# Performance work log

Hardware: AMD Instinct MI355X
Metric: run time of the kernel (lower is better)

## Reference

```python
import jax, jax.numpy as jnp
import numpy as np

B, N1, N2, D = 2, 512, 512, 128


def setup_inputs() -> dict:
    key = jax.random.key(0)
    ks = jax.random.split(key, 7)
    return {
        "x0": jax.random.normal(ks[0], (B, N1, D), dtype=jnp.float32),
        "x": jax.random.normal(ks[1], (B, N1, D), dtype=jnp.float32),
        "y": jax.random.normal(ks[2], (B, N2, D), dtype=jnp.float32),
        "W1": jax.random.normal(ks[3], (3 * D, D), dtype=jnp.float32) * (1.0 / np.sqrt(3 * D)),
        "b1": jax.random.normal(ks[4], (D,), dtype=jnp.float32) * 0.02,
        "W2": jax.random.normal(ks[5], (D, 1), dtype=jnp.float32) * (1.0 / np.sqrt(D)),
        "b2": jax.random.normal(ks[6], (1,), dtype=jnp.float32) * 0.02,
    }


def reference(x0, x, y, W1, b1, W2, b2):
    # linear1(concat([x0, x, y], -1)) == x0 @ W1[:D] + x @ W1[D:2D] + y @ W1[2D:] + b1
    d = x.shape[-1]
    Wa, Wb, Wc = W1[:d], W1[d:2 * d], W1[2 * d:]
    # small GEMMs on the un-expanded operands, then broadcast-add over the pair grid
    hx = jnp.einsum('bnd,de->bne', x0, Wa) + jnp.einsum('bnd,de->bne', x, Wb)  # [b, n1, d]
    hy = jnp.einsum('bmd,de->bme', y, Wc)                                      # [b, n2, d]
    h = hx[:, :, None, :] + hy[:, None, :, :] + b1                             # [b, n1, n2, d]
    h = jax.nn.gelu(h, approximate=False)                                      # torch nn.GELU default (erf)
    o = jnp.einsum('bnme,eo->bnmo', h, W2) + b2                                # [b, n1, n2, 1]
    return o[..., 0]                                                           # [b, n1, n2]
```

## Files before the change

kernel.cpp:

```cpp
#include <hip/hip_runtime.h>

#define BB 2
#define NN1 512
#define NN2 512
#define DD 128
#define TS 32
#define SXPAD 132

struct GeluPoly {
    float p[10];
    constexpr GeluPoly() : p{} {
        const int N = 10;
        const double PI = 3.14159265358979323846;
        double fv[10] = {};
        double xv[10] = {};
        for (int j = 0; j < N; ++j) {
            double th = PI * (j + 0.5) / N;
            double cth = 1.0, term = 1.0, t2 = th * th;
            for (int k = 1; k <= 30; ++k) {
                term *= -t2 / ((2.0 * k - 1.0) * (2.0 * k));
                cth += term;
            }
            xv[j] = cth;
            double t = 4.5 * (cth + 1.0);
            double s = t > 1.0 ? t : 1.0;
            for (int it = 0; it < 64; ++it) s = 0.5 * (s + t / s);
            double x = s * 0.70710678118654752440;
            double esum = 0.0, pw = x, fact = 1.0;
            for (int k = 0; k < 48; ++k) {
                if (k > 0) { fact *= (double)k; pw *= x * x; }
                double tk = pw / (fact * (2.0 * k + 1.0));
                esum += (k & 1) ? -tk : tk;
            }
            double erfv = 1.12837916709551257390 * esum;
            fv[j] = 0.5 * erfv / s;
        }
        double ck[10] = {};
        for (int k = 0; k < N; ++k) {
            double sum = 0.0;
            for (int j = 0; j < N; ++j) {
                double Tk = 1.0;
                if (k >= 1) {
                    double Tm2 = 1.0, Tm1 = xv[j];
                    Tk = xv[j];
                    for (int i = 2; i <= k; ++i) {
                        Tk = 2.0 * xv[j] * Tm1 - Tm2;
                        Tm2 = Tm1; Tm1 = Tk;
                    }
                }
                sum += fv[j] * Tk;
            }
            ck[k] = 2.0 * sum / N;
        }
        ck[0] *= 0.5;
        double T[10][10] = {};
        T[0][0] = 1.0;
        T[1][1] = 1.0;
        for (int k = 2; k < N; ++k)
            for (int i = 0; i < N; ++i)
                T[k][i] = 2.0 * (i > 0 ? T[k - 1][i - 1] : 0.0) - T[k - 2][i];
        double pd[10] = {};
        for (int k = 0; k < N; ++k)
            for (int i = 0; i < N; ++i)
                pd[i] += ck[k] * T[k][i];
        for (int i = 0; i < N; ++i) p[i] = (float)pd[i];
    }
};
static constexpr GeluPoly GP{};

__device__ __forceinline__ float gelu_poly(float s) {
    float c = __builtin_amdgcn_fmed3f(s, -3.0f, 3.0f);
    float t = c * c;
    float u = __builtin_fmaf(t, 0.22222222222222222f, -1.0f);
    float q = GP.p[9];
    #pragma unroll
    for (int k = 8; k >= 0; --k) q = __builtin_fmaf(q, u, GP.p[k]);
    float phi = __builtin_fmaf(c, q, 0.5f);
    return s * phi;
}

#define PR 8
__global__ __launch_bounds__(256) void proj_kernel(
    const float* __restrict__ x0, const float* __restrict__ x,
    const float* __restrict__ y,  const float* __restrict__ W1,
    const float* __restrict__ b1, float* __restrict__ hx, float* __restrict__ hy) {
    const int e = threadIdx.x & (DD - 1);
    const int g = threadIdx.x >> 7;
    const int nxb = (BB * NN1) / PR;
    const float* Wa = W1;
    const float* Wb = W1 + DD * DD;
    const float* Wc = W1 + 2 * DD * DD;

    if (blockIdx.x < nxb) {
        const int row0 = blockIdx.x * PR + g * (PR / 2);
        float acc0 = b1[e], acc1 = b1[e], acc2 = b1[e], acc3 = b1[e];
        #pragma unroll 4
        for (int d = 0; d < DD; ++d) {
            const float wa = Wa[d * DD + e];
            const float wb = Wb[d * DD + e];
            acc0 += x0[(row0 + 0) * DD + d] * wa + x[(row0 + 0) * DD + d] * wb;
            acc1 += x0[(row0 + 1) * DD + d] * wa + x[(row0 + 1) * DD + d] * wb;
            acc2 += x0[(row0 + 2) * DD + d] * wa + x[(row0 + 2) * DD + d] * wb;
            acc3 += x0[(row0 + 3) * DD + d] * wa + x[(row0 + 3) * DD + d] * wb;
        }
        hx[(row0 + 0) * DD + e] = acc0;
        hx[(row0 + 1) * DD + e] = acc1;
        hx[(row0 + 2) * DD + e] = acc2;
        hx[(row0 + 3) * DD + e] = acc3;
    } else {
        const int row0 = (blockIdx.x - nxb) * PR + g * (PR / 2);
        float acc0 = 0.f, acc1 = 0.f, acc2 = 0.f, acc3 = 0.f;
        #pragma unroll 4
        for (int d = 0; d < DD; ++d) {
            const float wc = Wc[d * DD + e];
            acc0 += y[(row0 + 0) * DD + d] * wc;
            acc1 += y[(row0 + 1) * DD + d] * wc;
            acc2 += y[(row0 + 2) * DD + d] * wc;
            acc3 += y[(row0 + 3) * DD + d] * wc;
        }
        hy[(row0 + 0) * DD + e] = acc0;
        hy[(row0 + 1) * DD + e] = acc1;
        hy[(row0 + 2) * DD + e] = acc2;
        hy[(row0 + 3) * DD + e] = acc3;
    }
}

__global__ __launch_bounds__(256) void cross_kernel(
    const float* __restrict__ hx, const float* __restrict__ hy,
    const float* __restrict__ W2, const float* __restrict__ b2,
    float* __restrict__ out) {
    __shared__ float sx[TS][SXPAD];
    __shared__ float sy[TS][SXPAD];
    __shared__ float sw[DD];

    const int b  = blockIdx.z;
    const int n0 = blockIdx.y * TS;
    const int m0 = blockIdx.x * TS;
    const int tid = threadIdx.x;

    for (int i = tid; i < TS * (DD / 4); i += 256) {
        const int r  = i >> 5;
        const int c4 = i & 31;
        *(float4*)&sx[r][c4 * 4] =
            *(const float4*)&hx[((b * NN1) + n0 + r) * DD + c4 * 4];
        *(float4*)&sy[r][c4 * 4] =
            *(const float4*)&hy[((b * NN2) + m0 + r) * DD + c4 * 4];
    }
    if (tid < DD) sw[tid] = W2[tid];
    __syncthreads();

    const int tn = (tid >> 4) * 2;
    const int tm = (tid & 15) * 2;

    float acc00 = 0.f, acc01 = 0.f, acc10 = 0.f, acc11 = 0.f;

    #pragma unroll 4
    for (int e4 = 0; e4 < DD / 4; ++e4) {
        const float4 a0 = *(const float4*)&sx[tn][e4 * 4];
        const float4 a1 = *(const float4*)&sx[tn + 1][e4 * 4];
        const float4 c0 = *(const float4*)&sy[tm][e4 * 4];
        const float4 c1 = *(const float4*)&sy[tm + 1][e4 * 4];
        const float4 w  = *(const float4*)&sw[e4 * 4];

        acc00 = __builtin_fmaf(gelu_poly(a0.x + c0.x), w.x, acc00);
        acc01 = __builtin_fmaf(gelu_poly(a0.x + c1.x), w.x, acc01);
        acc10 = __builtin_fmaf(gelu_poly(a1.x + c0.x), w.x, acc10);
        acc11 = __builtin_fmaf(gelu_poly(a1.x + c1.x), w.x, acc11);

        acc00 = __builtin_fmaf(gelu_poly(a0.y + c0.y), w.y, acc00);
        acc01 = __builtin_fmaf(gelu_poly(a0.y + c1.y), w.y, acc01);
        acc10 = __builtin_fmaf(gelu_poly(a1.y + c0.y), w.y, acc10);
        acc11 = __builtin_fmaf(gelu_poly(a1.y + c1.y), w.y, acc11);

        acc00 = __builtin_fmaf(gelu_poly(a0.z + c0.z), w.z, acc00);
        acc01 = __builtin_fmaf(gelu_poly(a0.z + c1.z), w.z, acc01);
        acc10 = __builtin_fmaf(gelu_poly(a1.z + c0.z), w.z, acc10);
        acc11 = __builtin_fmaf(gelu_poly(a1.z + c1.z), w.z, acc11);

        acc00 = __builtin_fmaf(gelu_poly(a0.w + c0.w), w.w, acc00);
        acc01 = __builtin_fmaf(gelu_poly(a0.w + c1.w), w.w, acc01);
        acc10 = __builtin_fmaf(gelu_poly(a1.w + c0.w), w.w, acc10);
        acc11 = __builtin_fmaf(gelu_poly(a1.w + c1.w), w.w, acc11);
    }

    const float bias = b2[0];
    float* o0 = &out[((size_t)(b * NN1) + n0 + tn) * NN2 + m0 + tm];
    float* o1 = o0 + NN2;
    *(float2*)o0 = make_float2(acc00 + bias, acc01 + bias);
    *(float2*)o1 = make_float2(acc10 + bias, acc11 + bias);
}

extern "C" void kernel_launch(void* const* d_in, const int* in_sizes, int n_in,
                              void* d_out, int out_size, void* d_ws, size_t ws_size,
                              hipStream_t stream) {
    const float* x0 = (const float*)d_in[0];
    const float* x  = (const float*)d_in[1];
    const float* y  = (const float*)d_in[2];
    const float* W1 = (const float*)d_in[3];
    const float* b1 = (const float*)d_in[4];
    const float* W2 = (const float*)d_in[5];
    const float* b2 = (const float*)d_in[6];
    float* out = (float*)d_out;

    float* hx = (float*)d_ws;
    float* hy = hx + (size_t)BB * NN1 * DD;

    const int nblocks = (BB * NN1) / PR + (BB * NN2) / PR;
    proj_kernel<<<nblocks, 256, 0, stream>>>(x0, x, y, W1, b1, hx, hy);
    cross_kernel<<<dim3(NN2 / TS, NN1 / TS, BB), 256, 0, stream>>>(hx, hy, W2, b2, out);
}
```

Measured before the change: 43.04 us.

## Shrink cross tile to 16x16 with one output per thread

Cuts the pair-grid tile from 32x32 to 16x16 and gives each thread a single output instead of a 2x2 micro-tile, with a serial accumulator over D. This launches four times as many blocks and reduces registers per thread, aiming for more occupancy and better load balance across CUs. In exchange each block reloads more hx/hy rows per output, the LDS reads per GELU evaluation double, and the single accumulator chain leaves less instruction-level parallelism. The float4 type is swapped for a clang vector type, which is cosmetic.

```diff
diff --git a/kernel.cpp b/kernel.cpp
--- a/kernel.cpp
+++ b/kernel.cpp
@@ -4,8 +4,10 @@
 #define NN1 512
 #define NN2 512
 #define DD 128
-#define TS 32
+#define TS 16
 #define SXPAD 132
+
+typedef float v4f __attribute__((ext_vector_type(4)));
 
 struct GeluPoly {
     float p[10];
@@ -75,8 +77,7 @@
     float q = GP.p[9];
     #pragma unroll
     for (int k = 8; k >= 0; --k) q = __builtin_fmaf(q, u, GP.p[k]);
-    float phi = __builtin_fmaf(c, q, 0.5f);
-    return s * phi;
+    return s * __builtin_fmaf(c, q, 0.5f);
 }
 
 #define PR 8
@@ -141,53 +142,30 @@
     for (int i = tid; i < TS * (DD / 4); i += 256) {
         const int r  = i >> 5;
         const int c4 = i & 31;
-        *(float4*)&sx[r][c4 * 4] =
-            *(const float4*)&hx[((b * NN1) + n0 + r) * DD + c4 * 4];
-        *(float4*)&sy[r][c4 * 4] =
-            *(const float4*)&hy[((b * NN2) + m0 + r) * DD + c4 * 4];
+        *(v4f*)&sx[r][c4 * 4] =
+            *(const v4f*)&hx[((b * NN1) + n0 + r) * DD + c4 * 4];
+        *(v4f*)&sy[r][c4 * 4] =
+            *(const v4f*)&hy[((b * NN2) + m0 + r) * DD + c4 * 4];
     }
     if (tid < DD) sw[tid] = W2[tid];
     __syncthreads();
 
-    const int tn = (tid >> 4) * 2;
-    const int tm = (tid & 15) * 2;
+    const int tn = tid >> 4;
+    const int tm = tid & 15;
 
-    float acc00 = 0.f, acc01 = 0.f, acc10 = 0.f, acc11 = 0.f;
-
-    #pragma unroll 4
+    float acc = 0.0f;
+    #pragma unroll 8
     for (int e4 = 0; e4 < DD / 4; ++e4) {
-        const float4 a0 = *(const float4*)&sx[tn][e4 * 4];
-        const float4 a1 = *(const float4*)&sx[tn + 1][e4 * 4];
-        const float4 c0 = *(const float4*)&sy[tm][e4 * 4];
-        const float4 c1 = *(const float4*)&sy[tm + 1][e4 * 4];
-        const float4 w  = *(const float4*)&sw[e4 * 4];
-
-        acc00 = __builtin_fmaf(gelu_poly(a0.x + c0.x), w.x, acc00);
-        acc01 = __builtin_fmaf(gelu_poly(a0.x + c1.x), w.x, acc01);
-        acc10 = __builtin_fmaf(gelu_poly(a1.x + c0.x), w.x, acc10);
-        acc11 = __builtin_fmaf(gelu_poly(a1.x + c1.x), w.x, acc11);
-
-        acc00 = __builtin_fmaf(gelu_poly(a0.y + c0.y), w.y, acc00);
-        acc01 = __builtin_fmaf(gelu_poly(a0.y + c1.y), w.y, acc01);
-        acc10 = __builtin_fmaf(gelu_poly(a1.y + c0.y), w.y, acc10);
-        acc11 = __builtin_fmaf(gelu_poly(a1.y + c1.y), w.y, acc11);
-
-        acc00 = __builtin_fmaf(gelu_poly(a0.z + c0.z), w.z, acc00);
-        acc01 = __builtin_fmaf(gelu_poly(a0.z + c1.z), w.z, acc01);
-        acc10 = __builtin_fmaf(gelu_poly(a1.z + c0.z), w.z, acc10);
-        acc11 = __builtin_fmaf(gelu_poly(a1.z + c1.z), w.z, acc11);
-
-        acc00 = __builtin_fmaf(gelu_poly(a0.w + c0.w), w.w, acc00);
-        acc01 = __builtin_fmaf(gelu_poly(a0.w + c1.w), w.w, acc01);
-        acc10 = __builtin_fmaf(gelu_poly(a1.w + c0.w), w.w, acc10);
-        acc11 = __builtin_fmaf(gelu_poly(a1.w + c1.w), w.w, acc11);
+        const v4f a = *(const v4f*)&sx[tn][e4 * 4];
+        const v4f c = *(const v4f*)&sy[tm][e4 * 4];
+        const v4f w = *(const v4f*)&sw[e4 * 4];
+        acc = __builtin_fmaf(gelu_poly(a.x + c.x), w.x, acc);
+        acc = __builtin_fmaf(gelu_poly(a.y + c.y), w.y, acc);
+        acc = __builtin_fmaf(gelu_poly(a.z + c.z), w.z, acc);
+        acc = __builtin_fmaf(gelu_poly(a.w + c.w), w.w, acc);
     }
 
-    const float bias = b2[0];
-    float* o0 = &out[((size_t)(b * NN1) + n0 + tn) * NN2 + m0 + tm];
-    float* o1 = o0 + NN2;
-    *(float2*)o0 = make_float2(acc00 + bias, acc01 + bias);
-    *(float2*)o1 = make_float2(acc10 + bias, acc11 + bias);
+    out[((size_t)(b * NN1) + n0 + tn) * NN2 + m0 + tm] = acc + b2[0];
 }
 
 extern "C" void kernel_launch(void* const* d_in, const int* in_sizes, int n_in,
```

New measurement: 41.44 us. 1.04x faster.
